# Optimization experiments

Measured on AMD Instinct MI355X. Metric: run time of the kernel, lower is better.

The kernel has to match this reference:

```python
import jax, jax.numpy as jnp
import numpy as np

U, I, D = 100000, 50000, 64
N = U + I
E = 3_000_000
B = 8192
NEG_SLOPE = 0.2
REG_LAMBDA = 1e-4


def setup_inputs() -> dict:
    key = jax.random.key(0)
    ks = jax.random.split(key, 16)
    s = 0.05  # xavier-ish scale for params
    inp = {
        "user": jax.random.randint(ks[0], (B,), 0, U, dtype=jnp.int32),
        "positive": jax.random.randint(ks[1], (B,), 0, I, dtype=jnp.int32),
        "negative": jax.random.randint(ks[2], (B,), 0, I, dtype=jnp.int32),
        "rows": jax.random.randint(ks[3], (E,), 0, N, dtype=jnp.int32),
        "cols": jax.random.randint(ks[4], (E,), 0, N, dtype=jnp.int32),
        # normalized adjacency values are small positive numbers ~ 1/sqrt(du*di)
        "vals": jax.random.uniform(ks[5], (E,), dtype=jnp.float32) * 0.05,
        "user_emb": jax.random.normal(ks[6], (U, D), dtype=jnp.float32) * s,
        "item_emb": jax.random.normal(ks[7], (I, D), dtype=jnp.float32) * s,
        "W_gcn0": jax.random.normal(ks[8], (D, D), dtype=jnp.float32) * s,
        "b_gcn0": jax.random.normal(ks[9], (1, D), dtype=jnp.float32) * s,
        "W_mlp0": jax.random.normal(ks[10], (D, D), dtype=jnp.float32) * s,
        "b_mlp0": jax.random.normal(ks[11], (1, D), dtype=jnp.float32) * s,
        "W_gcn1": jax.random.normal(ks[12], (D, D), dtype=jnp.float32) * s,
        "b_gcn1": jax.random.normal(ks[13], (1, D), dtype=jnp.float32) * s,
        "W_mlp1": jax.random.normal(ks[14], (D, D), dtype=jnp.float32) * s,
        "b_mlp1": jax.random.normal(ks[15], (1, D), dtype=jnp.float32) * s,
    }
    return inp


def reference(user, positive, negative, rows, cols, vals,
              user_emb, item_emb,
              W_gcn0, b_gcn0, W_mlp0, b_mlp0,
              W_gcn1, b_gcn1, W_mlp1, b_mlp1):
    def spmm(x):  # sparse (N,N) @ dense (N,D) via COO gather + segment-sum
        return jax.ops.segment_sum(vals[:, None] * x[cols], rows, num_segments=N)

    ego = jnp.concatenate([user_emb, item_emb], axis=0)  # [N, D]
    all_embs = [ego]
    for W_g, b_g, W_m, b_m in ((W_gcn0, b_gcn0, W_mlp0, b_mlp0),
                               (W_gcn1, b_gcn1, W_mlp1, b_mlp1)):
        side = spmm(ego)
        gcn = jax.nn.leaky_relu(side @ W_g + b_g, negative_slope=NEG_SLOPE)
        ego = gcn @ W_m + b_m  # mess_dropout prob = 0 -> identity
        norm = jnp.linalg.norm(ego, axis=1, keepdims=True)
        all_embs.append(ego / jnp.maximum(norm, 1e-12))  # F.normalize p=2
    final = jnp.concatenate(all_embs, axis=1)  # [N, 3*D]
    users_e, items_e = final[:U], final[U:]

    u = users_e[user]
    p = items_e[positive]
    n = items_e[negative]
    pos_s = jnp.sum(u * p, axis=-1)
    neg_s = jnp.sum(u * n, axis=-1)
    bpr_loss = jnp.mean(jax.nn.softplus(neg_s - pos_s))  # -mean(logsigmoid(pos-neg))

    eu = user_emb[user]
    ep = item_emb[positive]
    en = item_emb[negative]
    reg = 0.5 * (jnp.sum(eu ** 2) + jnp.sum(ep ** 2) + jnp.sum(en ** 2)) / B
    reg_loss = REG_LAMBDA * reg
    return jnp.stack([bpr_loss, reg_loss])
```

## Files before the change

kernel.cpp:

```cpp
#include <hip/hip_runtime.h>
#include <math.h>

#define U_CNT 100000
#define I_CNT 50000
#define D_DIM 64
#define N_CNT 150000
#define B_CNT 8192
#define NEG_SLOPE 0.2f
#define REG_LAMBDA 1e-4f

#define RPB 128
#define NBK ((N_CNT + RPB - 1) / RPB)
#define CAP 4096


__global__ __launch_bounds__(256) void k_bhist(const int* __restrict__ rows,
                                               int* __restrict__ bcnt, int E) {
    __shared__ int h[NBK];
    for (int i = threadIdx.x; i < NBK; i += 256) h[i] = 0;
    __syncthreads();
    int per = (E + gridDim.x - 1) / gridDim.x;
    int s = blockIdx.x * per, e = min(E, s + per);
    for (int i = s + threadIdx.x; i < e; i += 256) atomicAdd(&h[rows[i] >> 7], 1);
    __syncthreads();
    for (int i = threadIdx.x; i < NBK; i += 256) {
        int v = h[i];
        if (v) atomicAdd(&bcnt[i], v);
    }
}

__global__ void k_bscan(const int* __restrict__ bcnt, int* __restrict__ bb, int n) {
    __shared__ int lds[256];
    __shared__ int base;
    int tid = threadIdx.x;
    if (tid == 0) { base = 0; bb[0] = 0; }
    __syncthreads();
    for (int start = 0; start < n; start += 256) {
        int i = start + tid;
        int x = (i < n) ? bcnt[i] : 0;
        lds[tid] = x;
        __syncthreads();
        for (int off = 1; off < 256; off <<= 1) {
            int t = (tid >= off) ? lds[tid - off] : 0;
            __syncthreads();
            lds[tid] += t;
            __syncthreads();
        }
        if (i < n) bb[i + 1] = base + lds[tid];
        __syncthreads();
        if (tid == 0) base += lds[255];
        __syncthreads();
    }
}

__global__ __launch_bounds__(256) void k_bscatterA(const int* __restrict__ rows,
                                                   const int* __restrict__ cols,
                                                   const float* __restrict__ vals,
                                                   const int* __restrict__ bb,
                                                   int* __restrict__ bfill,
                                                   int2* __restrict__ edges, int E) {
    __shared__ int h[NBK];
    __shared__ int f[NBK];
    for (int i = threadIdx.x; i < NBK; i += 256) { h[i] = 0; f[i] = 0; }
    __syncthreads();
    int per = (E + gridDim.x - 1) / gridDim.x;
    int s = blockIdx.x * per, e = min(E, s + per);
    for (int i = s + threadIdx.x; i < e; i += 256) atomicAdd(&h[rows[i] >> 7], 1);
    __syncthreads();
    for (int i = threadIdx.x; i < NBK; i += 256) {
        int c = h[i];
        h[i] = c ? atomicAdd(&bfill[i], c) : 0;
    }
    __syncthreads();
    for (int i = s + threadIdx.x; i < e; i += 256) {
        int r = rows[i];
        int b = r >> 7, rl = r & 127;
        int pos = atomicAdd(&f[b], 1);
        int slot = bb[b] + h[b] + pos;
        edges[slot] = make_int2((rl << 18) | cols[i], __float_as_int(vals[i]));
    }
}

__global__ __launch_bounds__(256) void k_bfinal(int2* __restrict__ edges,
                                                const int* __restrict__ bb,
                                                int* __restrict__ rs, int E) {
    __shared__ int2 led[CAP];
    __shared__ int lcnt[RPB], lscan[RPB], lfill[RPB];
    int b = blockIdx.x;
    int s = bb[b], e = bb[b + 1];
    int nb = e - s;
    int tid = threadIdx.x;
    if (tid < RPB) { lcnt[tid] = 0; lfill[tid] = 0; }
    __syncthreads();
    for (int i = tid; i < nb; i += 256) {
        int2 ed = edges[s + i];
        if (i < CAP) led[i] = ed;
        atomicAdd(&lcnt[ed.x >> 18], 1);
    }
    __syncthreads();
    if (tid == 0) {
        int run = 0;
        for (int j = 0; j < RPB; ++j) { lscan[j] = run; run += lcnt[j]; }
    }
    __syncthreads();
    if (tid < RPB) {
        int row = b * RPB + tid;
        if (row < N_CNT) rs[row] = s + lscan[tid];
    }
    if (b == gridDim.x - 1 && tid == 0) rs[N_CNT] = E;
    int lim = min(nb, CAP);
    for (int i = tid; i < lim; i += 256) {
        int2 ed = led[i];
        int rl = ed.x >> 18;
        int pos = atomicAdd(&lfill[rl], 1);
        edges[s + lscan[rl] + pos] = make_int2(ed.x & 0x3FFFF, ed.y);
    }
    for (int base = CAP; base < nb; base += 256) {
        int i = base + tid;
        int2 ed;
        bool ok = (i < nb);
        if (ok) ed = edges[s + i];
        __syncthreads();
        if (ok) {
            int rl = ed.x >> 18;
            int pos = atomicAdd(&lfill[rl], 1);
            edges[s + lscan[rl] + pos] = make_int2(ed.x & 0x3FFFF, ed.y);
        }
        __syncthreads();
    }
}

__global__ void k_spmm(const int* __restrict__ rs, const int2* __restrict__ edges,
                       const float* __restrict__ srcA, const float* __restrict__ srcB,
                       int split, float* __restrict__ out) {
    int gid = blockIdx.x * blockDim.x + threadIdx.x;
    int w = gid >> 6;
    int lane = gid & 63;
    if (w >= N_CNT) return;
    int s = rs[w], e = rs[w + 1];
    float acc = 0.f;
    int i = s;
    for (; i + 4 <= e; i += 4) {
        int2 e0 = edges[i], e1 = edges[i + 1], e2 = edges[i + 2], e3 = edges[i + 3];
        const float* p0 = (e0.x < split) ? srcA + (size_t)e0.x * 64 : srcB + (size_t)(e0.x - split) * 64;
        const float* p1 = (e1.x < split) ? srcA + (size_t)e1.x * 64 : srcB + (size_t)(e1.x - split) * 64;
        const float* p2 = (e2.x < split) ? srcA + (size_t)e2.x * 64 : srcB + (size_t)(e2.x - split) * 64;
        const float* p3 = (e3.x < split) ? srcA + (size_t)e3.x * 64 : srcB + (size_t)(e3.x - split) * 64;
        float a0 = p0[lane], a1 = p1[lane], a2 = p2[lane], a3 = p3[lane];
        acc = fmaf(__int_as_float(e0.y), a0, acc);
        acc = fmaf(__int_as_float(e1.y), a1, acc);
        acc = fmaf(__int_as_float(e2.y), a2, acc);
        acc = fmaf(__int_as_float(e3.y), a3, acc);
    }
    for (; i < e; ++i) {
        int2 ed = edges[i];
        const float* p = (ed.x < split) ? srcA + (size_t)ed.x * 64 : srcB + (size_t)(ed.x - split) * 64;
        acc = fmaf(__int_as_float(ed.y), p[lane], acc);
    }
    out[(size_t)w * 64 + lane] = acc;
}

__global__ __launch_bounds__(256, 1) void k_dense(const float* __restrict__ x_in,
                                                  const float* __restrict__ Wg,
                                                  const float* __restrict__ bg,
                                                  const float* __restrict__ Wm,
                                                  const float* __restrict__ bm,
                                                  float* __restrict__ out,
                                                  float* __restrict__ rnorm) {
    __shared__ __align__(16) float sWgT[4096];
    __shared__ __align__(16) float sWm[4096];
    __shared__ float sbg[64], sbm[64];
    int tid = threadIdx.x;
    for (int i = tid; i < 4096; i += 256) {
        int k = i >> 6, j = i & 63;
        sWgT[j * 64 + k] = Wg[i];
        sWm[i] = Wm[i];
    }
    if (tid < 64) {
        sbg[tid] = bg[tid];
        sbm[tid] = bm[tid];
    }
    __syncthreads();
    int r = blockIdx.x * 256 + tid;
    if (r >= N_CNT) return;

    float4 x4[16];
    const float4* xp = (const float4*)(x_in + (size_t)r * 64);
#pragma unroll
    for (int i = 0; i < 16; ++i) x4[i] = xp[i];

    float z[64];
#pragma unroll
    for (int j = 0; j < 64; ++j) z[j] = sbm[j];

    for (int j = 0; j < 64; ++j) {
        float acc = sbg[j];
#pragma unroll
        for (int k = 0; k < 16; ++k) {
            float4 w = *(const float4*)&sWgT[j * 64 + k * 4];
            acc = fmaf(x4[k].x, w.x, acc);
            acc = fmaf(x4[k].y, w.y, acc);
            acc = fmaf(x4[k].z, w.z, acc);
            acc = fmaf(x4[k].w, w.w, acc);
        }
        float y = (acc >= 0.f) ? acc : NEG_SLOPE * acc;
#pragma unroll
        for (int k = 0; k < 16; ++k) {
            float4 w = *(const float4*)&sWm[j * 64 + k * 4];
            z[k * 4 + 0] = fmaf(y, w.x, z[k * 4 + 0]);
            z[k * 4 + 1] = fmaf(y, w.y, z[k * 4 + 1]);
            z[k * 4 + 2] = fmaf(y, w.z, z[k * 4 + 2]);
            z[k * 4 + 3] = fmaf(y, w.w, z[k * 4 + 3]);
        }
    }
    float nrm2 = 0.f;
#pragma unroll
    for (int j = 0; j < 64; ++j) nrm2 = fmaf(z[j], z[j], nrm2);
    float nrm = sqrtf(nrm2);
    float rn = 1.f / fmaxf(nrm, 1e-12f);
    rnorm[r] = rn;
    float4* op = (float4*)(out + (size_t)r * 64);
#pragma unroll
    for (int i = 0; i < 16; ++i) {
        float4 t;
        t.x = z[i * 4 + 0];
        t.y = z[i * 4 + 1];
        t.z = z[i * 4 + 2];
        t.w = z[i * 4 + 3];
        op[i] = t;
    }
}

#define SCORE_BLOCKS 128
__global__ __launch_bounds__(256) void k_score(const int* __restrict__ user,
                                               const int* __restrict__ posi,
                                               const int* __restrict__ negi,
                                               const float* __restrict__ uemb,
                                               const float* __restrict__ iemb,
                                               const float* __restrict__ ego1,
                                               const float* __restrict__ rn1,
                                               const float* __restrict__ ego2,
                                               const float* __restrict__ rn2,
                                               float* __restrict__ out) {
    __shared__ float ssp[4], srg[4];
    int tid = threadIdx.x;
    int lane = tid & 63;
    int wv = tid >> 6;
    int gw = blockIdx.x * 4 + wv;
    const int NW = SCORE_BLOCKS * 4;

    float sp_acc = 0.f, rg_acc = 0.f;
    for (int w = gw; w < B_CNT; w += NW) {
        int iu = user[w], ip = posi[w], ineg = negi[w];
        size_t ru = (size_t)iu;
        size_t rp = (size_t)U_CNT + ip;
        size_t rn_ = (size_t)U_CNT + ineg;

        float u0 = uemb[(size_t)iu * 64 + lane];
        float p0 = iemb[(size_t)ip * 64 + lane];
        float n0 = iemb[(size_t)ineg * 64 + lane];
        float pos = u0 * p0;
        float neg = u0 * n0;
        float reg = u0 * u0 + p0 * p0 + n0 * n0;

        float a1 = rn1[ru], b1 = rn1[rp], c1 = rn1[rn_];
        float u1 = ego1[ru * 64 + lane] * a1;
        float p1 = ego1[rp * 64 + lane] * b1;
        float n1 = ego1[rn_ * 64 + lane] * c1;
        pos = fmaf(u1, p1, pos);
        neg = fmaf(u1, n1, neg);

        float a2 = rn2[ru], b2 = rn2[rp], c2 = rn2[rn_];
        float u2 = ego2[ru * 64 + lane] * a2;
        float p2 = ego2[rp * 64 + lane] * b2;
        float n2 = ego2[rn_ * 64 + lane] * c2;
        pos = fmaf(u2, p2, pos);
        neg = fmaf(u2, n2, neg);

#pragma unroll
        for (int off = 32; off; off >>= 1) {
            pos += __shfl_xor(pos, off);
            neg += __shfl_xor(neg, off);
            reg += __shfl_xor(reg, off);
        }
        float t = neg - pos;
        float sp = fmaxf(t, 0.f) + log1pf(expf(-fabsf(t)));
        sp_acc += sp;
        rg_acc += reg;
    }
    if (lane == 0) {
        ssp[wv] = sp_acc;
        srg[wv] = rg_acc;
    }
    __syncthreads();
    if (tid == 0) {
        float s = ssp[0] + ssp[1] + ssp[2] + ssp[3];
        float r = srg[0] + srg[1] + srg[2] + srg[3];
        atomicAdd(&out[0], s * (1.0f / B_CNT));
        atomicAdd(&out[1], r * (0.5f * REG_LAMBDA / B_CNT));
    }
}


static inline size_t alignup(size_t x) { return (x + 255) & ~(size_t)255; }

extern "C" void kernel_launch(void* const* d_in, const int* in_sizes, int n_in,
                              void* d_out, int out_size, void* d_ws, size_t ws_size,
                              hipStream_t stream) {
    const int* user = (const int*)d_in[0];
    const int* posi = (const int*)d_in[1];
    const int* negi = (const int*)d_in[2];
    const int* rows = (const int*)d_in[3];
    const int* cols = (const int*)d_in[4];
    const float* vals = (const float*)d_in[5];
    const float* uemb = (const float*)d_in[6];
    const float* iemb = (const float*)d_in[7];
    const float* Wg0 = (const float*)d_in[8];
    const float* bg0 = (const float*)d_in[9];
    const float* Wm0 = (const float*)d_in[10];
    const float* bm0 = (const float*)d_in[11];
    const float* Wg1 = (const float*)d_in[12];
    const float* bg1 = (const float*)d_in[13];
    const float* Wm1 = (const float*)d_in[14];
    const float* bm1 = (const float*)d_in[15];
    const int E = in_sizes[3];
    float* out = (float*)d_out;

    char* p = (char*)d_ws;
    auto take = [&](size_t bytes) -> char* {
        char* q = p;
        p += alignup(bytes);
        return q;
    };
    int* rs = (int*)take((size_t)(N_CNT + 1) * 4);
    int* bcnt = (int*)take((size_t)NBK * 4 * 2);
    int* bfill = bcnt + NBK;
    int* bb = (int*)take((size_t)(NBK + 1) * 4);
    int2* edges = (int2*)take((size_t)E * 8);
    float* side = (float*)take((size_t)N_CNT * 64 * 4);
    float* ego1 = (float*)take((size_t)N_CNT * 64 * 4);
    float* ego2 = (float*)take((size_t)N_CNT * 64 * 4);
    float* rn1 = (float*)take((size_t)N_CNT * 4);
    float* rn2 = (float*)take((size_t)N_CNT * 4);

    hipMemsetAsync(out, 0, 2 * sizeof(float), stream);
    hipMemsetAsync(bcnt, 0, (size_t)NBK * 4 * 2, stream);

    k_bhist<<<256, 256, 0, stream>>>(rows, bcnt, E);
    k_bscan<<<1, 256, 0, stream>>>(bcnt, bb, NBK);
    k_bscatterA<<<256, 256, 0, stream>>>(rows, cols, vals, bb, bfill, edges, E);
    k_bfinal<<<NBK, 256, 0, stream>>>(edges, bb, rs, E);

    int sb = (N_CNT * 64 + 255) / 256;
    int db = (N_CNT + 255) / 256;

    k_spmm<<<sb, 256, 0, stream>>>(rs, edges, uemb, iemb, U_CNT, side);
    k_dense<<<db, 256, 0, stream>>>(side, Wg0, bg0, Wm0, bm0, ego1, rn1);
    k_spmm<<<sb, 256, 0, stream>>>(rs, edges, ego1, ego1, N_CNT, side);
    k_dense<<<db, 256, 0, stream>>>(side, Wg1, bg1, Wm1, bm1, ego2, rn2);

    k_score<<<SCORE_BLOCKS, 256, 0, stream>>>(user, posi, negi, uemb, iemb,
                                              ego1, rn1, ego2, rn2, out);
}
```

Baseline: 664.4 us.

## Store SpMM gather sources and intermediates in bf16 to halve gather bandwidth

Adds a conversion kernel that packs the concatenated user/item embeddings into bf16. SpMM now gathers bf16 rows and writes a bf16 side buffer, and the first dense kernel also emits a bf16 copy of ego1 for the second SpMM. The goal is to halve the bytes moved by the irregular 3M-edge gathers. The cost is an extra conversion pass plus extra writes, and bf16 rounding of the propagated features, which may hurt accuracy against the fp32 reference.

```diff
diff --git a/kernel.cpp b/kernel.cpp
--- a/kernel.cpp
+++ b/kernel.cpp
@@ -12,6 +12,32 @@
 #define RPB 128
 #define NBK ((N_CNT + RPB - 1) / RPB)
 #define CAP 4096
+
+__device__ __forceinline__ float bf2f(unsigned short u) {
+    return __uint_as_float((unsigned int)u << 16);
+}
+__device__ __forceinline__ unsigned short f2bf(float f) {
+    unsigned int x = __float_as_uint(f);
+    x += 0x7FFFu + ((x >> 16) & 1u);
+    return (unsigned short)(x >> 16);
+}
+
+__global__ __launch_bounds__(256) void k_cvt(const float* __restrict__ uemb,
+                                             const float* __restrict__ iemb,
+                                             unsigned short* __restrict__ dst) {
+    long long i = (long long)blockIdx.x * 256 + threadIdx.x;
+    long long base = i * 8;
+    const long long TOT = (long long)N_CNT * 64;
+    if (base >= TOT) return;
+    const long long USZ = (long long)U_CNT * 64;
+    const float* s = (base < USZ) ? uemb + base : iemb + (base - USZ);
+    float4 a = *(const float4*)s;
+    float4 b = *(const float4*)(s + 4);
+    union { unsigned short us[8]; uint4 v; } o;
+    o.us[0] = f2bf(a.x); o.us[1] = f2bf(a.y); o.us[2] = f2bf(a.z); o.us[3] = f2bf(a.w);
+    o.us[4] = f2bf(b.x); o.us[5] = f2bf(b.y); o.us[6] = f2bf(b.z); o.us[7] = f2bf(b.w);
+    *(uint4*)(dst + base) = o.v;
+}
 
 
 __global__ __launch_bounds__(256) void k_bhist(const int* __restrict__ rows,
@@ -131,8 +157,8 @@
 }
 
 __global__ void k_spmm(const int* __restrict__ rs, const int2* __restrict__ edges,
-                       const float* __restrict__ srcA, const float* __restrict__ srcB,
-                       int split, float* __restrict__ out) {
+                       const unsigned short* __restrict__ src,
+                       unsigned short* __restrict__ out_bf) {
     int gid = blockIdx.x * blockDim.x + threadIdx.x;
     int w = gid >> 6;
     int lane = gid & 63;
@@ -142,11 +168,10 @@
     int i = s;
     for (; i + 4 <= e; i += 4) {
         int2 e0 = edges[i], e1 = edges[i + 1], e2 = edges[i + 2], e3 = edges[i + 3];
-        const float* p0 = (e0.x < split) ? srcA + (size_t)e0.x * 64 : srcB + (size_t)(e0.x - split) * 64;
-        const float* p1 = (e1.x < split) ? srcA + (size_t)e1.x * 64 : srcB + (size_t)(e1.x - split) * 64;
-        const float* p2 = (e2.x < split) ? srcA + (size_t)e2.x * 64 : srcB + (size_t)(e2.x - split) * 64;
-        const float* p3 = (e3.x < split) ? srcA + (size_t)e3.x * 64 : srcB + (size_t)(e3.x - split) * 64;
-        float a0 = p0[lane], a1 = p1[lane], a2 = p2[lane], a3 = p3[lane];
+        float a0 = bf2f(src[e0.x * 64 + lane]);
+        float a1 = bf2f(src[e1.x * 64 + lane]);
+        float a2 = bf2f(src[e2.x * 64 + lane]);
+        float a3 = bf2f(src[e3.x * 64 + lane]);
         acc = fmaf(__int_as_float(e0.y), a0, acc);
         acc = fmaf(__int_as_float(e1.y), a1, acc);
         acc = fmaf(__int_as_float(e2.y), a2, acc);
@@ -154,18 +179,19 @@
     }
     for (; i < e; ++i) {
         int2 ed = edges[i];
-        const float* p = (ed.x < split) ? srcA + (size_t)ed.x * 64 : srcB + (size_t)(ed.x - split) * 64;
-        acc = fmaf(__int_as_float(ed.y), p[lane], acc);
-    }
-    out[(size_t)w * 64 + lane] = acc;
-}
-
-__global__ __launch_bounds__(256, 1) void k_dense(const float* __restrict__ x_in,
+        acc = fmaf(__int_as_float(ed.y), bf2f(src[ed.x * 64 + lane]), acc);
+    }
+    out_bf[(size_t)w * 64 + lane] = f2bf(acc);
+}
+
+template <int WRITE_BF>
+__global__ __launch_bounds__(256, 1) void k_dense(const unsigned short* __restrict__ x_in,
                                                   const float* __restrict__ Wg,
                                                   const float* __restrict__ bg,
                                                   const float* __restrict__ Wm,
                                                   const float* __restrict__ bm,
                                                   float* __restrict__ out,
+                                                  unsigned short* __restrict__ out_bf,
                                                   float* __restrict__ rnorm) {
     __shared__ __align__(16) float sWgT[4096];
     __shared__ __align__(16) float sWm[4096];
@@ -184,10 +210,17 @@
     int r = blockIdx.x * 256 + tid;
     if (r >= N_CNT) return;
 
-    float4 x4[16];
-    const float4* xp = (const float4*)(x_in + (size_t)r * 64);
-#pragma unroll
-    for (int i = 0; i < 16; ++i) x4[i] = xp[i];
+    float xr[64];
+    const uint4* xp = (const uint4*)(x_in + (size_t)r * 64);
+#pragma unroll
+    for (int t = 0; t < 8; ++t) {
+        uint4 q = xp[t];
+        unsigned int u;
+        u = q.x; xr[t * 8 + 0] = __uint_as_float(u << 16); xr[t * 8 + 1] = __uint_as_float(u & 0xFFFF0000u);
+        u = q.y; xr[t * 8 + 2] = __uint_as_float(u << 16); xr[t * 8 + 3] = __uint_as_float(u & 0xFFFF0000u);
+        u = q.z; xr[t * 8 + 4] = __uint_as_float(u << 16); xr[t * 8 + 5] = __uint_as_float(u & 0xFFFF0000u);
+        u = q.w; xr[t * 8 + 6] = __uint_as_float(u << 16); xr[t * 8 + 7] = __uint_as_float(u & 0xFFFF0000u);
+    }
 
     float z[64];
 #pragma unroll
@@ -198,10 +231,10 @@
 #pragma unroll
         for (int k = 0; k < 16; ++k) {
             float4 w = *(const float4*)&sWgT[j * 64 + k * 4];
-            acc = fmaf(x4[k].x, w.x, acc);
-            acc = fmaf(x4[k].y, w.y, acc);
-            acc = fmaf(x4[k].z, w.z, acc);
-            acc = fmaf(x4[k].w, w.w, acc);
+            acc = fmaf(xr[k * 4 + 0], w.x, acc);
+            acc = fmaf(xr[k * 4 + 1], w.y, acc);
+            acc = fmaf(xr[k * 4 + 2], w.z, acc);
+            acc = fmaf(xr[k * 4 + 3], w.w, acc);
         }
         float y = (acc >= 0.f) ? acc : NEG_SLOPE * acc;
 #pragma unroll
@@ -228,6 +261,16 @@
         t.z = z[i * 4 + 2];
         t.w = z[i * 4 + 3];
         op[i] = t;
+    }
+    if (WRITE_BF) {
+        uint4* bp = (uint4*)(out_bf + (size_t)r * 64);
+#pragma unroll
+        for (int t = 0; t < 8; ++t) {
+            union { unsigned short us[8]; uint4 v; } o;
+#pragma unroll
+            for (int q = 0; q < 8; ++q) o.us[q] = f2bf(z[t * 8 + q]);
+            bp[t] = o.v;
+        }
     }
 }
 
@@ -337,7 +380,9 @@
     int* bfill = bcnt + NBK;
     int* bb = (int*)take((size_t)(NBK + 1) * 4);
     int2* edges = (int2*)take((size_t)E * 8);
-    float* side = (float*)take((size_t)N_CNT * 64 * 4);
+    unsigned short* ego0_bf = (unsigned short*)take((size_t)N_CNT * 64 * 2);
+    unsigned short* side_bf = (unsigned short*)take((size_t)N_CNT * 64 * 2);
+    unsigned short* ego1_bf = (unsigned short*)take((size_t)N_CNT * 64 * 2);
     float* ego1 = (float*)take((size_t)N_CNT * 64 * 4);
     float* ego2 = (float*)take((size_t)N_CNT * 64 * 4);
     float* rn1 = (float*)take((size_t)N_CNT * 4);
@@ -346,6 +391,10 @@
     hipMemsetAsync(out, 0, 2 * sizeof(float), stream);
     hipMemsetAsync(bcnt, 0, (size_t)NBK * 4 * 2, stream);
 
+    const long long TOT = (long long)N_CNT * 64;
+    int cb = (int)((TOT / 8 + 255) / 256);
+    k_cvt<<<cb, 256, 0, stream>>>(uemb, iemb, ego0_bf);
+
     k_bhist<<<256, 256, 0, stream>>>(rows, bcnt, E);
     k_bscan<<<1, 256, 0, stream>>>(bcnt, bb, NBK);
     k_bscatterA<<<256, 256, 0, stream>>>(rows, cols, vals, bb, bfill, edges, E);
@@ -354,10 +403,10 @@
     int sb = (N_CNT * 64 + 255) / 256;
     int db = (N_CNT + 255) / 256;
 
-    k_spmm<<<sb, 256, 0, stream>>>(rs, edges, uemb, iemb, U_CNT, side);
-    k_dense<<<db, 256, 0, stream>>>(side, Wg0, bg0, Wm0, bm0, ego1, rn1);
-    k_spmm<<<sb, 256, 0, stream>>>(rs, edges, ego1, ego1, N_CNT, side);
-    k_dense<<<db, 256, 0, stream>>>(side, Wg1, bg1, Wm1, bm1, ego2, rn2);
+    k_spmm<<<sb, 256, 0, stream>>>(rs, edges, ego0_bf, side_bf);
+    k_dense<1><<<db, 256, 0, stream>>>(side_bf, Wg0, bg0, Wm0, bm0, ego1, ego1_bf, rn1);
+    k_spmm<<<sb, 256, 0, stream>>>(rs, edges, ego1_bf, side_bf);
+    k_dense<0><<<db, 256, 0, stream>>>(side_bf, Wg1, bg1, Wm1, bm1, ego2, (unsigned short*)nullptr, rn2);
 
     k_score<<<SCORE_BLOCKS, 256, 0, stream>>>(user, posi, negi, uemb, iemb,
                                               ego1, rn1, ego2, rn2, out);
```

Result: faster. 637.9 us (-4.0%).
